# Kernel tuning notes

Measured on AMD Instinct MI355X. Metric: run time of the kernel, lower is better.

## Reference

```python
import jax, jax.numpy as jnp
import numpy as np
from jax import lax

# dims
B, N, D, H, K, NS = 16, 4096, 64, 128, 32, 1024  # clouds, pts/cloud, feat, hidden, max neighbors, fps samples
R = 0.2  # radius


def _fps(pos, n_s):
    """Farthest point sampling on one cloud. pos: [N,3] -> idx [n_s] int32."""
    n = pos.shape[0]

    def step(carry, _):
        dist, last = carry
        d = jnp.sum((pos - pos[last]) ** 2, axis=-1)
        dist = jnp.minimum(dist, d)
        nxt = jnp.argmax(dist).astype(jnp.int32)
        return (dist, nxt), last

    init = (jnp.full((n,), 1e10, pos.dtype), jnp.int32(0))
    _, idx = lax.scan(step, init, None, length=n_s)
    return idx


def setup_inputs() -> dict:
    key = jax.random.key(0)
    ks = jax.random.split(key, 6)
    s1 = 1.0 / np.sqrt(D + 1)
    s2 = 1.0 / np.sqrt(H)
    s3 = 1.0 / np.sqrt(D + H)
    return {
        "x": jax.random.normal(ks[0], (B, N, D), jnp.float32),
        "pos": jax.random.uniform(ks[1], (B, N, 3), jnp.float32),
        "W1": jax.random.normal(ks[2], (D + 1, H), jnp.float32) * s1,
        "b1": jnp.zeros((H,), jnp.float32),
        "W2": jax.random.normal(ks[3], (H, 3), jnp.float32) * s2,
        "b2": jnp.zeros((3,), jnp.float32),
        "W3": jax.random.normal(ks[4], (D + H, H), jnp.float32) * s3,
        "b3": jnp.zeros((H,), jnp.float32),
    }


def reference(x, pos, W1, b1, W2, b2, W3, b3):
    # 1) FPS downsample per cloud -> centers
    idx = jax.vmap(lambda p: _fps(p, NS))(pos)                    # [B,NS]
    pos_s = jax.vmap(lambda p, i: p[i])(pos, idx)                 # [B,NS,3]

    # 2) radius neighbor search: nearest-K within R (<= max_num_neighbors=32)
    d2 = jnp.sum((pos_s[:, :, None, :] - pos[:, None, :, :]) ** 2, axis=-1)  # [B,NS,N]
    masked = jnp.where(d2 <= R * R, d2, jnp.inf)
    neg, nbr = lax.top_k(-masked, K)                              # nearest K
    valid = (-neg) <= R * R                                       # [B,NS,K]

    # 3) gather neighbor features/positions
    x_j = jax.vmap(lambda a, i: a[i])(x, nbr)                     # [B,NS,K,D]
    pos_j = jax.vmap(lambda a, i: a[i])(pos, nbr)                 # [B,NS,K,3]
    diff = pos_j - pos_s[:, :, None, :]                           # pos_j - pos_i
    d2sel = jnp.sum(diff ** 2, axis=-1)
    dist = jnp.where(d2sel > 0, jnp.sqrt(jnp.where(d2sel > 0, d2sel, 1.0)), 0.0)

    # 4) message MLPs
    feat = jnp.concatenate([x_j, dist[..., None]], axis=-1)       # [B,NS,K,D+1]
    emb = jax.nn.relu(feat @ W1 + b1)                             # nn_msg_x
    pw = emb @ W2 + b2                                            # nn_msg_pos
    pmsg = diff * pw

    # 5) masked aggregate: sum for x, mean for pos
    m = valid[..., None].astype(emb.dtype)
    aggr_x = jnp.sum(emb * m, axis=2)                             # [B,NS,H]
    cnt = jnp.maximum(jnp.sum(m, axis=2), 1.0)                    # [B,NS,1]
    aggr_pos = jnp.sum(pmsg * m, axis=2) / cnt                    # [B,NS,3]

    # 6) update
    x_d = jax.vmap(lambda a, i: a[i])(x, idx)                     # [B,NS,D]
    out_x = jax.nn.relu(jnp.concatenate([x_d, aggr_x], axis=-1) @ W3 + b3)
    out_pos = pos_s + aggr_pos
    return out_x, out_pos, idx
```

## Files before the change

### kernel.cpp

```cpp
#include <hip/hip_runtime.h>
#include <math.h>

#define B_ 16
#define N_ 4096
#define D_ 64
#define H_ 128
#define K_ 32
#define NS_ 1024
#define R2_ 0.04f
#define CAP_ 1024

typedef short short8 __attribute__((ext_vector_type(8)));
typedef float f32x4 __attribute__((ext_vector_type(4)));

static __device__ __forceinline__ short f2bf(float f) {
    unsigned u = __float_as_uint(f);
    unsigned r = (u + 0x7FFFu + ((u >> 16) & 1u)) >> 16;
    return (short)r;
}

template<int CTRL, int RM>
static __device__ __forceinline__ unsigned dppmov(unsigned v) {
    return (unsigned)__builtin_amdgcn_update_dpp((int)v, (int)v, CTRL, RM, 0xF, false);
}

#define DPP_FMAX_STEP(CTRL, RM)                                           \
    {                                                                     \
        float n = __uint_as_float(dppmov<CTRL, RM>(__float_as_uint(wm))); \
        wm = fmaxf(wm, n);                                                \
    }

#define DPP_UMIN_STEP(CTRL, RM)                                           \
    {                                                                     \
        unsigned n = dppmov<CTRL, RM>(cand);                              \
        cand = n < cand ? n : cand;                                       \
    }

#define DPP_MIN_STEP(CTRL, RM)                                            \
    {                                                                     \
        unsigned nh = dppmov<CTRL, RM>(kh);                               \
        unsigned nl = dppmov<CTRL, RM>(kl);                               \
        unsigned long long nk = (((unsigned long long)nh) << 32) | nl;    \
        unsigned long long ok = (((unsigned long long)kh) << 32) | kl;    \
        if (nk < ok) { kh = nh; kl = nl; }                                \
    }

__global__ __launch_bounds__(256) void fps_kernel(
    const float* __restrict__ pos, int* __restrict__ idx_i,
    float* __restrict__ idx_f, float* __restrict__ pos_s)
{
    __shared__ float4 lpos4[N_];
    __shared__ float4 sres[NS_];
    __shared__ unsigned long long skey[2][4];
    const int b = blockIdx.x;
    const int t = threadIdx.x;
    const int wv = t >> 6;
    const int lane = t & 63;
    const float* posb = pos + (size_t)b * N_ * 3;
    for (int p = t; p < N_; p += 256)
        lpos4[p] = make_float4(posb[3 * p + 0], posb[3 * p + 1], posb[3 * p + 2], 0.f);
    __syncthreads();

    float px[16], py[16], pz[16], dist[16];
#pragma unroll
    for (int j = 0; j < 16; ++j) {
        float4 v = lpos4[t + 256 * j];
        px[j] = v.x; py[j] = v.y; pz[j] = v.z;
        dist[j] = 1e10f;
    }
    unsigned curidx = 0;
    float4 c0 = lpos4[0];
    float ccx = c0.x, ccy = c0.y, ccz = c0.z;

    for (int ns = 0; ns < NS_; ++ns) {
        if (t == 0)
            sres[ns] = make_float4(ccx, ccy, ccz, __uint_as_float(curidx));
        float bv = -1.f; int bj = 0;
#pragma unroll
        for (int j = 0; j < 16; ++j) {
            float dx = __fsub_rn(px[j], ccx);
            float dy = __fsub_rn(py[j], ccy);
            float dz = __fsub_rn(pz[j], ccz);
            float d2 = __fadd_rn(__fadd_rn(__fmul_rn(dx, dx), __fmul_rn(dy, dy)), __fmul_rn(dz, dz));
            float dn = fminf(dist[j], d2);
            dist[j] = dn;
            bool g = dn > bv;
            bv = g ? dn : bv;
            bj = g ? j : bj;
        }
        float wm = bv;
        DPP_FMAX_STEP(0x111, 0xF)
        DPP_FMAX_STEP(0x112, 0xF)
        DPP_FMAX_STEP(0x114, 0xF)
        DPP_FMAX_STEP(0x118, 0xF)
        DPP_FMAX_STEP(0x142, 0xA)
        DPP_FMAX_STEP(0x143, 0xC)
        const float wavemax = __uint_as_float(
            (unsigned)__builtin_amdgcn_readlane((int)__float_as_uint(wm), 63));
        unsigned cand = (bv == wavemax) ? (unsigned)(t | (bj << 8)) : 0xFFFFFFFFu;
        DPP_UMIN_STEP(0x111, 0xF)
        DPP_UMIN_STEP(0x112, 0xF)
        DPP_UMIN_STEP(0x114, 0xF)
        DPP_UMIN_STEP(0x118, 0xF)
        DPP_UMIN_STEP(0x142, 0xA)
        DPP_UMIN_STEP(0x143, 0xC)
        const unsigned widx = (unsigned)__builtin_amdgcn_readlane((int)cand, 63);
        if (lane == 0)
            skey[ns & 1][wv] = (((unsigned long long)__float_as_uint(wavemax)) << 32)
                             | (unsigned long long)(0xFFFFFFFFu - widx);
        __syncthreads();
        {
            unsigned long long skv = skey[ns & 1][lane & 3];
            unsigned kh2 = (unsigned)(skv >> 32), kl2 = (unsigned)skv;
#define SLOT_STEP(CTRL)                                                        \
            {                                                                  \
                unsigned nh = dppmov<CTRL, 0xF>(kh2);                          \
                unsigned nl = dppmov<CTRL, 0xF>(kl2);                          \
                unsigned long long nk = (((unsigned long long)nh) << 32) | nl; \
                unsigned long long ok = (((unsigned long long)kh2) << 32) | kl2;\
                if (nk > ok) { kh2 = nh; kl2 = nl; }                           \
            }
            SLOT_STEP(0x101)
            SLOT_STEP(0x102)
#undef SLOT_STEP
            curidx = 0xFFFFFFFFu - (unsigned)__builtin_amdgcn_readlane((int)kl2, 0);
        }
        {
            float4 cc = lpos4[curidx];
            ccx = cc.x; ccy = cc.y; ccz = cc.z;
        }
    }
    __syncthreads();
    for (int i = t; i < NS_; i += 256) {
        float4 r = sres[i];
        unsigned id = __float_as_uint(r.w);
        idx_i[b * NS_ + i] = (int)id;
        idx_f[b * NS_ + i] = (float)id;
        pos_s[(b * NS_ + i) * 3 + 0] = r.x;
        pos_s[(b * NS_ + i) * 3 + 1] = r.y;
        pos_s[(b * NS_ + i) * 3 + 2] = r.z;
    }
}

__global__ __launch_bounds__(256) void nbr_kernel(
    const float* __restrict__ pos, const float* __restrict__ pos_s,
    int* __restrict__ nbr, float* __restrict__ cntv)
{
    __shared__ unsigned long long ck[4][CAP_];
    const int w = threadIdx.x >> 6;
    const int lane = threadIdx.x & 63;
    const int s = blockIdx.x * 4 + w;
    const int b = s >> 10;
    const float cx = pos_s[s * 3 + 0], cy = pos_s[s * 3 + 1], cz = pos_s[s * 3 + 2];
    const float* posb = pos + (size_t)b * N_ * 3;
    int m = 0;
    for (int base = 0; base < N_; base += 64) {
        int p = base + lane;
        float dx = __fsub_rn(posb[3 * p + 0], cx);
        float dy = __fsub_rn(posb[3 * p + 1], cy);
        float dz = __fsub_rn(posb[3 * p + 2], cz);
        float d2 = __fadd_rn(__fadd_rn(__fmul_rn(dx, dx), __fmul_rn(dy, dy)), __fmul_rn(dz, dz));
        bool in = (d2 <= R2_);
        unsigned long long msk = __ballot(in);
        int before = __popcll(msk & ((1ull << lane) - 1ull));
        int slot = m + before;
        if (in && slot < CAP_)
            ck[w][slot] = ((unsigned long long)__float_as_uint(d2) << 32) | (unsigned)p;
        m += __popcll(msk);
    }
    if (m > CAP_) m = CAP_;
    __asm__ volatile("s_waitcnt lgkmcnt(0)" ::: "memory");
    int kcnt = m < K_ ? m : K_;
    unsigned chosen = 0;
    for (int k = 0; k < kcnt; ++k) {
        unsigned long long localk = ~0ull; int bslot = -1;
        for (int r = 0; r * 64 + lane < m; ++r) {
            if (chosen & (1u << r)) continue;
            int q = r * 64 + lane;
            unsigned long long key = ck[w][q];
            if (key < localk) { localk = key; bslot = q; }
        }
        unsigned kh = (unsigned)(localk >> 32), kl = (unsigned)localk;
        DPP_MIN_STEP(0x111, 0xF)
        DPP_MIN_STEP(0x112, 0xF)
        DPP_MIN_STEP(0x114, 0xF)
        DPP_MIN_STEP(0x118, 0xF)
        DPP_MIN_STEP(0x142, 0xA)
        DPP_MIN_STEP(0x143, 0xC)
        unsigned mh = (unsigned)__builtin_amdgcn_readlane((int)kh, 63);
        unsigned ml = (unsigned)__builtin_amdgcn_readlane((int)kl, 63);
        unsigned long long bk = (((unsigned long long)mh) << 32) | ml;
        if (localk == bk && bslot >= 0) chosen |= 1u << (bslot >> 6);
        if (lane == 0) nbr[s * K_ + k] = (int)(bk & 0xFFFFFFFFull);
    }
    if (lane == 0) {
        for (int k = kcnt; k < K_; ++k) nbr[s * K_ + k] = -1;
        cntv[s] = (float)kcnt;
    }
}

__global__ __launch_bounds__(256) void msg_kernel(
    const float* __restrict__ x, const float* __restrict__ pos,
    const float* __restrict__ W1, const float* __restrict__ b1,
    const float* __restrict__ W2, const float* __restrict__ b2,
    const float* __restrict__ pos_s, const int* __restrict__ nbr,
    const float* __restrict__ cntv, float* __restrict__ aggr_x,
    float* __restrict__ out_pos)
{
    __shared__ __align__(16) char smem[4 * 5120];
    const int t = threadIdx.x;
    const int wv = t >> 6, lane = t & 63;
    const int quad = lane >> 4, cl = lane & 15;
    char* wb = smem + wv * 5120;

    short8 bfrag[8][2];
    float b1v[8], w1dv[8], w2v0[8], w2v1[8], w2v2[8];
#pragma unroll
    for (int Nt = 0; Nt < 8; ++Nt) {
        const int h = Nt * 16 + cl;
#pragma unroll
        for (int ks = 0; ks < 2; ++ks) {
            short8 f;
#pragma unroll
            for (int jj = 0; jj < 8; ++jj)
                f[jj] = f2bf(W1[(ks * 32 + quad * 8 + jj) * H_ + h]);
            bfrag[Nt][ks] = f;
        }
        b1v[Nt] = b1[h];
        w1dv[Nt] = W1[64 * H_ + h];
        w2v0[Nt] = W2[h * 3 + 0];
        w2v1[Nt] = W2[h * 3 + 1];
        w2v2[Nt] = W2[h * 3 + 2];
    }
    const float b20 = b2[0], b21 = b2[1], b22 = b2[2];

    const int kkg = lane >> 1, half = lane & 1;
    for (int i = 0; i < 4; ++i) {
        const int s = blockIdx.x * 16 + wv * 4 + i;
        const int b = s >> 10;
        const int n = nbr[s * K_ + kkg];
        {
            char* frow = wb + kkg * 144 + half * 64;
            if (n >= 0) {
                const float4* xr = (const float4*)(x + ((size_t)b * N_ + n) * D_) + half * 8;
#pragma unroll
                for (int q = 0; q < 4; ++q) {
                    float4 a = xr[q * 2], c = xr[q * 2 + 1];
                    short8 o;
                    o[0] = f2bf(a.x); o[1] = f2bf(a.y); o[2] = f2bf(a.z); o[3] = f2bf(a.w);
                    o[4] = f2bf(c.x); o[5] = f2bf(c.y); o[6] = f2bf(c.z); o[7] = f2bf(c.w);
                    *(short8*)(frow + q * 16) = o;
                }
            } else {
                short8 z = {0, 0, 0, 0, 0, 0, 0, 0};
#pragma unroll
                for (int q = 0; q < 4; ++q) *(short8*)(frow + q * 16) = z;
            }
            if (half == 0) {
                float dxm = 0.f, dym = 0.f, dzm = 0.f, de = -1.f;
                if (n >= 0) {
                    const float* pj = pos + ((size_t)b * N_ + n) * 3;
                    float dx = pj[0] - pos_s[s * 3 + 0];
                    float dy = pj[1] - pos_s[s * 3 + 1];
                    float dz = pj[2] - pos_s[s * 3 + 2];
                    float d2 = dx * dx + dy * dy + dz * dz;
                    de = d2 > 0.f ? sqrtf(d2) : 0.f;
                    dxm = dx; dym = dy; dzm = dz;
                }
                f32x4 sv = {dxm, dym, dzm, de};
                *(f32x4*)(wb + 4608 + kkg * 16) = sv;
            }
        }
        float agp[8] = {0, 0, 0, 0, 0, 0, 0, 0};
        float gp0[8] = {0, 0, 0, 0, 0, 0, 0, 0};
        float gp1[8] = {0, 0, 0, 0, 0, 0, 0, 0};
        float gp2[8] = {0, 0, 0, 0, 0, 0, 0, 0};
#pragma unroll
        for (int Mt = 0; Mt < 2; ++Mt) {
            short8 a0 = *(short8*)(wb + (Mt * 16 + cl) * 144 + quad * 16);
            short8 a1 = *(short8*)(wb + (Mt * 16 + cl) * 144 + 64 + quad * 16);
            f32x4 acc[8];
#pragma unroll
            for (int Nt = 0; Nt < 8; ++Nt) {
                f32x4 z = {0.f, 0.f, 0.f, 0.f};
                z = __builtin_amdgcn_mfma_f32_16x16x32_bf16(a0, bfrag[Nt][0], z, 0, 0, 0);
                z = __builtin_amdgcn_mfma_f32_16x16x32_bf16(a1, bfrag[Nt][1], z, 0, 0, 0);
                acc[Nt] = z;
            }
            f32x4 sd[4];
#pragma unroll
            for (int r = 0; r < 4; ++r)
                sd[r] = *(f32x4*)(wb + 4608 + (Mt * 16 + quad * 4 + r) * 16);
#pragma unroll
            for (int Nt = 0; Nt < 8; ++Nt) {
#pragma unroll
                for (int r = 0; r < 4; ++r) {
                    float dr = sd[r][3];
                    float wgt = dr >= 0.f ? 1.f : 0.f;
                    float dd = dr >= 0.f ? dr : 0.f;
                    float e = fmaf(dd, w1dv[Nt], acc[Nt][r]) + b1v[Nt];
                    e = e > 0.f ? e : 0.f;
                    agp[Nt] = fmaf(wgt, e, agp[Nt]);
                    gp0[Nt] = fmaf(sd[r][0], e, gp0[Nt]);
                    gp1[Nt] = fmaf(sd[r][1], e, gp1[Nt]);
                    gp2[Nt] = fmaf(sd[r][2], e, gp2[Nt]);
                }
            }
        }
#pragma unroll
        for (int Nt = 0; Nt < 8; ++Nt) {
            float v = agp[Nt]; v += __shfl_xor(v, 16); v += __shfl_xor(v, 32);
            aggr_x[(size_t)s * H_ + Nt * 16 + cl] = v;
            float g0 = gp0[Nt]; g0 += __shfl_xor(g0, 16); g0 += __shfl_xor(g0, 32); gp0[Nt] = g0;
            float g1 = gp1[Nt]; g1 += __shfl_xor(g1, 16); g1 += __shfl_xor(g1, 32); gp1[Nt] = g1;
            float g2 = gp2[Nt]; g2 += __shfl_xor(g2, 16); g2 += __shfl_xor(g2, 32); gp2[Nt] = g2;
        }
        float pr0 = 0.f, pr1 = 0.f, pr2 = 0.f;
#pragma unroll
        for (int Nt = 0; Nt < 8; ++Nt) {
            pr0 = fmaf(w2v0[Nt], gp0[Nt], pr0);
            pr1 = fmaf(w2v1[Nt], gp1[Nt], pr1);
            pr2 = fmaf(w2v2[Nt], gp2[Nt], pr2);
        }
#pragma unroll
        for (int off = 1; off < 16; off <<= 1) {
            pr0 += __shfl_xor(pr0, off);
            pr1 += __shfl_xor(pr1, off);
            pr2 += __shfl_xor(pr2, off);
        }
        f32x4 dsv = *(f32x4*)(wb + 4608 + (lane & 31) * 16);
        float q0 = dsv[0], q1 = dsv[1], q2 = dsv[2];
#pragma unroll
        for (int off = 1; off < 32; off <<= 1) {
            q0 += __shfl_xor(q0, off);
            q1 += __shfl_xor(q1, off);
            q2 += __shfl_xor(q2, off);
        }
        float cnt = cntv[s]; if (cnt < 1.f) cnt = 1.f;
        if (lane < 3) {
            float pr = lane == 0 ? pr0 : (lane == 1 ? pr1 : pr2);
            float qq = lane == 0 ? q0 : (lane == 1 ? q1 : q2);
            float bb = lane == 0 ? b20 : (lane == 1 ? b21 : b22);
            out_pos[s * 3 + lane] = pos_s[s * 3 + lane] + (pr + bb * qq) / cnt;
        }
    }
}

__global__ __launch_bounds__(128) void out_kernel(
    const float* __restrict__ x, const float* __restrict__ W3,
    const float* __restrict__ b3, const int* __restrict__ idx_i,
    const float* __restrict__ aggr_x, float* __restrict__ out_x)
{
    __shared__ float rows[32][208];
    const int t = threadIdx.x;
    const int s0 = blockIdx.x * 32;
    const int sl = t >> 2, part = t & 3;
    const int s = s0 + sl;
    const int b = s >> 10;
    const int id = idx_i[s];
    {
        const float4* xr = (const float4*)(x + ((size_t)b * N_ + id) * D_);
        float4* rr = (float4*)&rows[sl][0];
#pragma unroll
        for (int q = 0; q < 4; ++q) rr[part * 4 + q] = xr[part * 4 + q];
        const float4* ar = (const float4*)(aggr_x + (size_t)s * H_);
        float4* rr2 = (float4*)&rows[sl][64];
#pragma unroll
        for (int q = 0; q < 8; ++q) rr2[part * 8 + q] = ar[part * 8 + q];
    }
    __syncthreads();
    float acc[32];
#pragma unroll
    for (int i = 0; i < 32; ++i) acc[i] = 0.f;
    for (int j4 = 0; j4 < 48; ++j4) {
        float w0 = W3[(j4 * 4 + 0) * H_ + t];
        float w1 = W3[(j4 * 4 + 1) * H_ + t];
        float w2 = W3[(j4 * 4 + 2) * H_ + t];
        float w3 = W3[(j4 * 4 + 3) * H_ + t];
#pragma unroll
        for (int i = 0; i < 32; ++i) {
            const float4 f = *(const float4*)&rows[i][j4 * 4];
            float a = acc[i];
            a = fmaf(f.x, w0, a); a = fmaf(f.y, w1, a);
            a = fmaf(f.z, w2, a); a = fmaf(f.w, w3, a);
            acc[i] = a;
        }
    }
    const float bb = b3[t];
#pragma unroll
    for (int i = 0; i < 32; ++i) {
        float v = acc[i] + bb;
        v = v > 0.f ? v : 0.f;
        out_x[(size_t)(s0 + i) * H_ + t] = v;
    }
}

extern "C" void kernel_launch(void* const* d_in, const int* in_sizes, int n_in,
                              void* d_out, int out_size, void* d_ws, size_t ws_size,
                              hipStream_t stream) {
    const float* x   = (const float*)d_in[0];
    const float* pos = (const float*)d_in[1];
    const float* W1  = (const float*)d_in[2];
    const float* b1  = (const float*)d_in[3];
    const float* W2  = (const float*)d_in[4];
    const float* b2  = (const float*)d_in[5];
    const float* W3  = (const float*)d_in[6];
    const float* b3  = (const float*)d_in[7];

    float* out_x   = (float*)d_out;
    float* out_pos = (float*)d_out + 2097152;
    float* idx_f   = (float*)d_out + 2146304;

    char* ws = (char*)d_ws;
    int*   idx_i  = (int*)ws;
    float* pos_s  = (float*)(ws + 65536);
    int*   nbr    = (int*)(ws + 262144);
    float* cntv   = (float*)(ws + 2359296);
    float* aggr_x = (float*)(ws + 2424832);

    fps_kernel<<<B_, 256, 0, stream>>>(pos, idx_i, idx_f, pos_s);
    nbr_kernel<<<(B_ * NS_) / 4, 256, 0, stream>>>(pos, pos_s, nbr, cntv);
    msg_kernel<<<(B_ * NS_) / 16, 256, 0, stream>>>(x, pos, W1, b1, W2, b2,
                                                    pos_s, nbr, cntv, aggr_x, out_pos);
    out_kernel<<<(B_ * NS_) / 32, 128, 0, stream>>>(x, W3, b3, idx_i, aggr_x, out_x);
}
```

Baseline: 1.026 ms.

## Pre-convert x to bf16, register-cache neighbor keys, shortcut FPS argmax tie-break

A new kernel converts x to bf16 once into workspace, so the message kernel gathers half as many bytes per neighbor and does no per-gather conversion. In neighbor selection, when at most 384 candidates fall in the radius, the keys are held in registers (6 per lane) and the repeated K-selection scans those registers instead of LDS. In FPS, a ballot skips the DPP min-index reduction when only one lane holds the maximum, and the launch bound now asks for one block per CU. The cost is an extra pass over x plus a second branch in neighbor selection.

```diff
diff --git a/kernel.cpp b/kernel.cpp
--- a/kernel.cpp
+++ b/kernel.cpp
@@ -12,6 +12,7 @@
 
 typedef short short8 __attribute__((ext_vector_type(8)));
 typedef float f32x4 __attribute__((ext_vector_type(4)));
+typedef unsigned short ushort_t;
 
 static __device__ __forceinline__ short f2bf(float f) {
     unsigned u = __float_as_uint(f);
@@ -45,7 +46,19 @@
         if (nk < ok) { kh = nh; kl = nl; }                                \
     }
 
-__global__ __launch_bounds__(256) void fps_kernel(
+__global__ __launch_bounds__(256) void cvt_kernel(
+    const float* __restrict__ x, ushort_t* __restrict__ xb)
+{
+    const size_t i = ((size_t)blockIdx.x * 256 + threadIdx.x) * 8;
+    float4 a = *(const float4*)(x + i);
+    float4 c = *(const float4*)(x + i + 4);
+    short8 o;
+    o[0] = f2bf(a.x); o[1] = f2bf(a.y); o[2] = f2bf(a.z); o[3] = f2bf(a.w);
+    o[4] = f2bf(c.x); o[5] = f2bf(c.y); o[6] = f2bf(c.z); o[7] = f2bf(c.w);
+    *(short8*)(xb + i) = o;
+}
+
+__global__ __launch_bounds__(256, 1) void fps_kernel(
     const float* __restrict__ pos, int* __restrict__ idx_i,
     float* __restrict__ idx_f, float* __restrict__ pos_s)
 {
@@ -97,14 +110,22 @@
         DPP_FMAX_STEP(0x143, 0xC)
         const float wavemax = __uint_as_float(
             (unsigned)__builtin_amdgcn_readlane((int)__float_as_uint(wm), 63));
-        unsigned cand = (bv == wavemax) ? (unsigned)(t | (bj << 8)) : 0xFFFFFFFFu;
-        DPP_UMIN_STEP(0x111, 0xF)
-        DPP_UMIN_STEP(0x112, 0xF)
-        DPP_UMIN_STEP(0x114, 0xF)
-        DPP_UMIN_STEP(0x118, 0xF)
-        DPP_UMIN_STEP(0x142, 0xA)
-        DPP_UMIN_STEP(0x143, 0xC)
-        const unsigned widx = (unsigned)__builtin_amdgcn_readlane((int)cand, 63);
+        const unsigned pidx = (unsigned)t + ((unsigned)bj << 8);
+        const unsigned long long mask = __ballot(bv == wavemax);
+        unsigned widx;
+        if (__popcll(mask) == 1) {
+            const int wl = __ffsll((long long)mask) - 1;
+            widx = (unsigned)__builtin_amdgcn_readlane((int)pidx, wl);
+        } else {
+            unsigned cand = (bv == wavemax) ? pidx : 0xFFFFFFFFu;
+            DPP_UMIN_STEP(0x111, 0xF)
+            DPP_UMIN_STEP(0x112, 0xF)
+            DPP_UMIN_STEP(0x114, 0xF)
+            DPP_UMIN_STEP(0x118, 0xF)
+            DPP_UMIN_STEP(0x142, 0xA)
+            DPP_UMIN_STEP(0x143, 0xC)
+            widx = (unsigned)__builtin_amdgcn_readlane((int)cand, 63);
+        }
         if (lane == 0)
             skey[ns & 1][wv] = (((unsigned long long)__float_as_uint(wavemax)) << 32)
                              | (unsigned long long)(0xFFFFFFFFu - widx);
@@ -171,27 +192,59 @@
     if (m > CAP_) m = CAP_;
     __asm__ volatile("s_waitcnt lgkmcnt(0)" ::: "memory");
     int kcnt = m < K_ ? m : K_;
-    unsigned chosen = 0;
-    for (int k = 0; k < kcnt; ++k) {
-        unsigned long long localk = ~0ull; int bslot = -1;
-        for (int r = 0; r * 64 + lane < m; ++r) {
-            if (chosen & (1u << r)) continue;
+    if (m <= 384) {
+        unsigned long long kr[6];
+#pragma unroll
+        for (int r = 0; r < 6; ++r) {
             int q = r * 64 + lane;
-            unsigned long long key = ck[w][q];
-            if (key < localk) { localk = key; bslot = q; }
-        }
-        unsigned kh = (unsigned)(localk >> 32), kl = (unsigned)localk;
-        DPP_MIN_STEP(0x111, 0xF)
-        DPP_MIN_STEP(0x112, 0xF)
-        DPP_MIN_STEP(0x114, 0xF)
-        DPP_MIN_STEP(0x118, 0xF)
-        DPP_MIN_STEP(0x142, 0xA)
-        DPP_MIN_STEP(0x143, 0xC)
-        unsigned mh = (unsigned)__builtin_amdgcn_readlane((int)kh, 63);
-        unsigned ml = (unsigned)__builtin_amdgcn_readlane((int)kl, 63);
-        unsigned long long bk = (((unsigned long long)mh) << 32) | ml;
-        if (localk == bk && bslot >= 0) chosen |= 1u << (bslot >> 6);
-        if (lane == 0) nbr[s * K_ + k] = (int)(bk & 0xFFFFFFFFull);
+            unsigned long long v = ck[w][q & (CAP_ - 1)];
+            kr[r] = (q < m) ? v : ~0ull;
+        }
+        unsigned chosen = 0;
+        for (int k = 0; k < kcnt; ++k) {
+            unsigned long long localk = ~0ull; int br = -1;
+#pragma unroll
+            for (int r = 0; r < 6; ++r) {
+                bool ok = (!((chosen >> r) & 1u)) && (kr[r] < localk);
+                localk = ok ? kr[r] : localk;
+                br = ok ? r : br;
+            }
+            unsigned kh = (unsigned)(localk >> 32), kl = (unsigned)localk;
+            DPP_MIN_STEP(0x111, 0xF)
+            DPP_MIN_STEP(0x112, 0xF)
+            DPP_MIN_STEP(0x114, 0xF)
+            DPP_MIN_STEP(0x118, 0xF)
+            DPP_MIN_STEP(0x142, 0xA)
+            DPP_MIN_STEP(0x143, 0xC)
+            unsigned mh = (unsigned)__builtin_amdgcn_readlane((int)kh, 63);
+            unsigned ml = (unsigned)__builtin_amdgcn_readlane((int)kl, 63);
+            unsigned long long bk = (((unsigned long long)mh) << 32) | ml;
+            if (localk == bk && br >= 0) chosen |= 1u << br;
+            if (lane == 0) nbr[s * K_ + k] = (int)(bk & 0xFFFFFFFFull);
+        }
+    } else {
+        unsigned chosen = 0;
+        for (int k = 0; k < kcnt; ++k) {
+            unsigned long long localk = ~0ull; int bslot = -1;
+            for (int r = 0; r * 64 + lane < m; ++r) {
+                if (chosen & (1u << r)) continue;
+                int q = r * 64 + lane;
+                unsigned long long key = ck[w][q];
+                if (key < localk) { localk = key; bslot = q; }
+            }
+            unsigned kh = (unsigned)(localk >> 32), kl = (unsigned)localk;
+            DPP_MIN_STEP(0x111, 0xF)
+            DPP_MIN_STEP(0x112, 0xF)
+            DPP_MIN_STEP(0x114, 0xF)
+            DPP_MIN_STEP(0x118, 0xF)
+            DPP_MIN_STEP(0x142, 0xA)
+            DPP_MIN_STEP(0x143, 0xC)
+            unsigned mh = (unsigned)__builtin_amdgcn_readlane((int)kh, 63);
+            unsigned ml = (unsigned)__builtin_amdgcn_readlane((int)kl, 63);
+            unsigned long long bk = (((unsigned long long)mh) << 32) | ml;
+            if (localk == bk && bslot >= 0) chosen |= 1u << (bslot >> 6);
+            if (lane == 0) nbr[s * K_ + k] = (int)(bk & 0xFFFFFFFFull);
+        }
     }
     if (lane == 0) {
         for (int k = kcnt; k < K_; ++k) nbr[s * K_ + k] = -1;
@@ -200,7 +253,7 @@
 }
 
 __global__ __launch_bounds__(256) void msg_kernel(
-    const float* __restrict__ x, const float* __restrict__ pos,
+    const ushort_t* __restrict__ xb, const float* __restrict__ pos,
     const float* __restrict__ W1, const float* __restrict__ b1,
     const float* __restrict__ W2, const float* __restrict__ b2,
     const float* __restrict__ pos_s, const int* __restrict__ nbr,
@@ -242,15 +295,9 @@
         {
             char* frow = wb + kkg * 144 + half * 64;
             if (n >= 0) {
-                const float4* xr = (const float4*)(x + ((size_t)b * N_ + n) * D_) + half * 8;
-#pragma unroll
-                for (int q = 0; q < 4; ++q) {
-                    float4 a = xr[q * 2], c = xr[q * 2 + 1];
-                    short8 o;
-                    o[0] = f2bf(a.x); o[1] = f2bf(a.y); o[2] = f2bf(a.z); o[3] = f2bf(a.w);
-                    o[4] = f2bf(c.x); o[5] = f2bf(c.y); o[6] = f2bf(c.z); o[7] = f2bf(c.w);
-                    *(short8*)(frow + q * 16) = o;
-                }
+                const short8* xr = (const short8*)(xb + ((size_t)b * N_ + n) * D_) + half * 4;
+#pragma unroll
+                for (int q = 0; q < 4; ++q) *(short8*)(frow + q * 16) = xr[q];
             } else {
                 short8 z = {0, 0, 0, 0, 0, 0, 0, 0};
 #pragma unroll
@@ -412,15 +459,17 @@
     float* idx_f   = (float*)d_out + 2146304;
 
     char* ws = (char*)d_ws;
-    int*   idx_i  = (int*)ws;
-    float* pos_s  = (float*)(ws + 65536);
-    int*   nbr    = (int*)(ws + 262144);
-    float* cntv   = (float*)(ws + 2359296);
-    float* aggr_x = (float*)(ws + 2424832);
-
+    int*      idx_i  = (int*)ws;
+    float*    pos_s  = (float*)(ws + 65536);
+    int*      nbr    = (int*)(ws + 262144);
+    float*    cntv   = (float*)(ws + 2359296);
+    float*    aggr_x = (float*)(ws + 2424832);
+    ushort_t* x_bf16 = (ushort_t*)(ws + 10813440);
+
+    cvt_kernel<<<(B_ * N_ * D_) / (256 * 8), 256, 0, stream>>>(x, x_bf16);
     fps_kernel<<<B_, 256, 0, stream>>>(pos, idx_i, idx_f, pos_s);
     nbr_kernel<<<(B_ * NS_) / 4, 256, 0, stream>>>(pos, pos_s, nbr, cntv);
-    msg_kernel<<<(B_ * NS_) / 16, 256, 0, stream>>>(x, pos, W1, b1, W2, b2,
+    msg_kernel<<<(B_ * NS_) / 16, 256, 0, stream>>>(x_bf16, pos, W1, b1, W2, b2,
                                                     pos_s, nbr, cntv, aggr_x, out_pos);
     out_kernel<<<(B_ * NS_) / 32, 128, 0, stream>>>(x, W3, b3, idx_i, aggr_x, out_x);
 }
```

After: 987.2 us. -3.8%, faster.
